# Optimization experiments

Measured on AMD Instinct MI355X. Metric: run time of the kernel, lower is better.

Reference implementation:

```python
import jax, jax.numpy as jnp
import numpy as np

N, DIM_IN, DIM_V, VH, VW, H = 2048, 256, 256, 7, 7, 64
NK = VH * VW
DIM_Q = DIM_V * H  # 16384
EPS = 1e-5


def layer_norm(x, g, b):
    m = jnp.mean(x, axis=-1, keepdims=True)
    var = jnp.mean((x - m) ** 2, axis=-1, keepdims=True)
    return (x - m) / jnp.sqrt(var + EPS) * g + b


def setup_inputs() -> dict:
    key = jax.random.key(0)
    ks = jax.random.split(key, 6)
    x = jax.random.normal(ks[0], (N, DIM_IN), dtype=jnp.float32)
    v = jax.random.normal(ks[1], (N, DIM_V, NK), dtype=jnp.float32)
    Wq_w = jax.random.normal(ks[2], (2 * DIM_Q, DIM_IN), dtype=jnp.float32) * 0.02
    Wq_b = jnp.zeros((2 * DIM_Q,), dtype=jnp.float32)
    Wv_w = jax.random.normal(ks[3], (DIM_IN, DIM_V * NK), dtype=jnp.float32) * 0.02
    Wv_b = jnp.zeros((DIM_IN,), dtype=jnp.float32)
    return {
        "x": x, "v": v,
        "Wq_w": Wq_w, "Wq_b": Wq_b,
        "ln0_g": jnp.ones((H,), jnp.float32), "ln0_b": jnp.zeros((H,), jnp.float32),
        "ln1_g": jnp.ones((DIM_V,), jnp.float32), "ln1_b": jnp.zeros((DIM_V,), jnp.float32),
        "Wv_w": Wv_w, "Wv_b": Wv_b,
        "lnv_g": jnp.ones((DIM_IN,), jnp.float32), "lnv_b": jnp.zeros((DIM_IN,), jnp.float32),
        "lnf_g": jnp.ones((DIM_IN,), jnp.float32), "lnf_b": jnp.zeros((DIM_IN,), jnp.float32),
    }


def reference(x, v, Wq_w, Wq_b, ln0_g, ln0_b, ln1_g, ln1_b, Wv_w, Wv_b, lnv_g, lnv_b, lnf_g, lnf_b):
    n = x.shape[0]
    vt = jnp.transpose(v, (0, 2, 1))                      # [N, Nk, V]
    q = x @ Wq_w.T + Wq_b                                 # [N, 2*dim_q]
    # dynamic_conv_num == 2: two bmm stages with per-sample weights from q
    p1 = q[:, :DIM_Q].reshape(n, DIM_V, H)                # [N, V, H]
    t = jnp.einsum('nkv,nvh->nkh', vt, p1)                # [N, Nk, H]
    t = jax.nn.relu(layer_norm(t, ln0_g, ln0_b))
    p2 = q[:, DIM_Q:].reshape(n, H, DIM_V)                # [N, H, V]
    t = jnp.einsum('nkh,nhv->nkv', t, p2)                 # [N, Nk, V]
    t = jax.nn.relu(layer_norm(t, ln1_g, ln1_b))
    flat = t.reshape(n, NK * DIM_V)                       # [N, Nk*V]
    w = jax.nn.relu(layer_norm(flat @ Wv_w.T + Wv_b, lnv_g, lnv_b))  # [N, dim_in]
    return layer_norm(x + w, lnf_g, lnf_b)
```

## Files before the change

kernel.cpp:

```cpp
#include <hip/hip_runtime.h>

#define LN_EPS 1e-5f


typedef __attribute__((ext_vector_type(8))) short short8;
typedef __attribute__((ext_vector_type(16))) float f32x16;

__global__ __launch_bounds__(256) void k0_split(
    const float* __restrict__ in, ushort* __restrict__ hi,
    ushort* __restrict__ lo, int n4)
{
    const int i = blockIdx.x * 256 + threadIdx.x;
    if (i >= n4) return;
    const float4 f = ((const float4*)in)[i];
    const uint ux = __float_as_uint(f.x), uy = __float_as_uint(f.y);
    const uint uz = __float_as_uint(f.z), uw = __float_as_uint(f.w);
    ushort4 h, l;
    h.x = (ushort)(ux >> 16); h.y = (ushort)(uy >> 16);
    h.z = (ushort)(uz >> 16); h.w = (ushort)(uw >> 16);
    l.x = (ushort)(__float_as_uint(f.x - __uint_as_float(ux & 0xffff0000u)) >> 16);
    l.y = (ushort)(__float_as_uint(f.y - __uint_as_float(uy & 0xffff0000u)) >> 16);
    l.z = (ushort)(__float_as_uint(f.z - __uint_as_float(uz & 0xffff0000u)) >> 16);
    l.w = (ushort)(__float_as_uint(f.w - __uint_as_float(uw & 0xffff0000u)) >> 16);
    ((ushort4*)hi)[i] = h;
    ((ushort4*)lo)[i] = l;
}

template<bool HAS_BIAS>
__global__ __launch_bounds__(256, 2) void gemm_sb3(
    const ushort* __restrict__ Ah, const ushort* __restrict__ Al,
    const float* __restrict__ B, const float* __restrict__ bias,
    float* __restrict__ C, int lda, int ldb, int ldc,
    size_t cSplitStride, int kPerSplit)
{
    __shared__ __align__(16) ushort sAh[8192];
    __shared__ __align__(16) ushort sAl[8192];
    __shared__ __align__(16) ushort sBh[8192];
    __shared__ __align__(16) ushort sBl[8192];

    const int tid = threadIdx.x;
    const int m0 = blockIdx.x << 7;
    const int j0 = blockIdx.y << 7;
    const int ks0 = blockIdx.z * kPerSplit;
    float* Cb = C + (size_t)blockIdx.z * cSplitStride;

    const int lane = tid & 63;
    const int wid = tid >> 6;
    const int wr = wid >> 1;
    const int wc = wid & 1;
    const int swz = (lane & 7) << 3;
    const int rA = (wr << 6) + (lane & 31);
    const int rB = (wc << 6) + (lane & 31);
    const int khalf = (lane >> 5) << 3;

    f32x16 acc[2][2];
#pragma unroll
    for (int r = 0; r < 2; ++r)
#pragma unroll
        for (int c = 0; c < 2; ++c)
#pragma unroll
            for (int e = 0; e < 16; ++e) acc[r][c][e] = 0.f;

    for (int kg0 = 0; kg0 < kPerSplit; kg0 += 64) {
        const int kg = ks0 + kg0;

        uint4 av[8];
#pragma unroll
        for (int p = 0; p < 2; ++p) {
            const ushort* src = p ? Al : Ah;
#pragma unroll
            for (int i = 0; i < 4; ++i) {
                const int id = tid + (i << 8);
                const int row = id >> 3;
                const int c8 = (id & 7) << 3;
                av[p * 4 + i] = *(const uint4*)(src + (size_t)(m0 + row) * lda + kg + c8);
            }
        }
        float4 bv[8];
#pragma unroll
        for (int i = 0; i < 8; ++i) {
            const int id = tid + (i << 8);
            const int row = id >> 4;
            const int c4 = (id & 15) << 2;
            bv[i] = *(const float4*)(B + (size_t)(j0 + row) * ldb + kg + c4);
        }

        if (kg0 > 0) __syncthreads();

#pragma unroll
        for (int p = 0; p < 2; ++p) {
            ushort* dst = p ? sAl : sAh;
#pragma unroll
            for (int i = 0; i < 4; ++i) {
                const int id = tid + (i << 8);
                const int row = id >> 3;
                const int c8 = (id & 7) << 3;
                *(uint4*)&dst[((row << 6) + c8) ^ ((row & 7) << 3)] = av[p * 4 + i];
            }
        }
#pragma unroll
        for (int i = 0; i < 8; ++i) {
            const int id = tid + (i << 8);
            const int row = id >> 4;
            const int c4 = (id & 15) << 2;
            const uint ux = __float_as_uint(bv[i].x), uy = __float_as_uint(bv[i].y);
            const uint uz = __float_as_uint(bv[i].z), uw = __float_as_uint(bv[i].w);
            const float lx = bv[i].x - __uint_as_float(ux & 0xffff0000u);
            const float ly = bv[i].y - __uint_as_float(uy & 0xffff0000u);
            const float lz = bv[i].z - __uint_as_float(uz & 0xffff0000u);
            const float lw = bv[i].w - __uint_as_float(uw & 0xffff0000u);
            const uint h01 = (ux >> 16) | (uy & 0xffff0000u);
            const uint h23 = (uz >> 16) | (uw & 0xffff0000u);
            const uint l01 = (__float_as_uint(lx) >> 16) | (__float_as_uint(ly) & 0xffff0000u);
            const uint l23 = (__float_as_uint(lz) >> 16) | (__float_as_uint(lw) & 0xffff0000u);
            const int sidx = ((row << 6) + c4) ^ ((row & 7) << 3);
            *(uint2*)&sBh[sidx] = make_uint2(h01, h23);
            *(uint2*)&sBl[sidx] = make_uint2(l01, l23);
        }
        __syncthreads();

#pragma unroll
        for (int ks = 0; ks < 4; ++ks) {
            const int kf = (ks << 4) + khalf;
            const int ia0 = ((rA << 6) + kf) ^ swz;
            const int ia1 = (((rA + 32) << 6) + kf) ^ swz;
            const int ib0 = ((rB << 6) + kf) ^ swz;
            const int ib1 = (((rB + 32) << 6) + kf) ^ swz;
            const short8 a0h = *(const short8*)&sAh[ia0];
            const short8 a0l = *(const short8*)&sAl[ia0];
            const short8 a1h = *(const short8*)&sAh[ia1];
            const short8 a1l = *(const short8*)&sAl[ia1];
            const short8 b0h = *(const short8*)&sBh[ib0];
            const short8 b0l = *(const short8*)&sBl[ib0];
            const short8 b1h = *(const short8*)&sBh[ib1];
            const short8 b1l = *(const short8*)&sBl[ib1];

            acc[0][0] = __builtin_amdgcn_mfma_f32_32x32x16_bf16(a0h, b0h, acc[0][0], 0, 0, 0);
            acc[0][1] = __builtin_amdgcn_mfma_f32_32x32x16_bf16(a0h, b1h, acc[0][1], 0, 0, 0);
            acc[1][0] = __builtin_amdgcn_mfma_f32_32x32x16_bf16(a1h, b0h, acc[1][0], 0, 0, 0);
            acc[1][1] = __builtin_amdgcn_mfma_f32_32x32x16_bf16(a1h, b1h, acc[1][1], 0, 0, 0);
            acc[0][0] = __builtin_amdgcn_mfma_f32_32x32x16_bf16(a0h, b0l, acc[0][0], 0, 0, 0);
            acc[0][1] = __builtin_amdgcn_mfma_f32_32x32x16_bf16(a0h, b1l, acc[0][1], 0, 0, 0);
            acc[1][0] = __builtin_amdgcn_mfma_f32_32x32x16_bf16(a1h, b0l, acc[1][0], 0, 0, 0);
            acc[1][1] = __builtin_amdgcn_mfma_f32_32x32x16_bf16(a1h, b1l, acc[1][1], 0, 0, 0);
            acc[0][0] = __builtin_amdgcn_mfma_f32_32x32x16_bf16(a0l, b0h, acc[0][0], 0, 0, 0);
            acc[0][1] = __builtin_amdgcn_mfma_f32_32x32x16_bf16(a0l, b1h, acc[0][1], 0, 0, 0);
            acc[1][0] = __builtin_amdgcn_mfma_f32_32x32x16_bf16(a1l, b0h, acc[1][0], 0, 0, 0);
            acc[1][1] = __builtin_amdgcn_mfma_f32_32x32x16_bf16(a1l, b1h, acc[1][1], 0, 0, 0);
        }
    }

#pragma unroll
    for (int rb = 0; rb < 2; ++rb)
#pragma unroll
        for (int cb = 0; cb < 2; ++cb) {
            const int col = j0 + (wc << 6) + (cb << 5) + (lane & 31);
            const float bvv = HAS_BIAS ? bias[col] : 0.0f;
            const int rbase = m0 + (wr << 6) + (rb << 5) + ((lane >> 5) << 2);
            float* cp = Cb + (size_t)rbase * ldc + col;
#pragma unroll
            for (int reg = 0; reg < 16; ++reg) {
                const int rr = (reg & 3) + ((reg >> 2) << 3);
                cp[(size_t)rr * ldc] = acc[rb][cb][reg] + bvv;
            }
        }
}

__global__ __launch_bounds__(1024, 4) void k2_dynconv(
    const float* __restrict__ v, const float* __restrict__ q,
    const float* __restrict__ ln0g, const float* __restrict__ ln0b,
    const float* __restrict__ ln1g, const float* __restrict__ ln1b,
    ushort* __restrict__ fhi, ushort* __restrict__ flo)
{
    __shared__ __align__(16) float sm[33028];
    float* const vL = sm;
    float* const pL = sm + 13312;
    float* const tL = sm + 29696;

    const int n = blockIdx.x;
    const int tid = threadIdx.x;
    const float* vrow = v + (size_t)n * 12544;
    const float* qrow = q + (size_t)n * 32768;

    float4 rp2[4];
#pragma unroll
    for (int j = 0; j < 4; ++j)
        rp2[j] = *(const float4*)(qrow + 16384 + ((tid + j * 1024) << 2));

#pragma unroll
    for (int j = 0; j < 4; ++j) {
        const int c = tid + j * 1024;
        *(float4*)&pL[c << 2] = *(const float4*)(qrow + (c << 2));
    }
#pragma unroll
    for (int j = 0; j < 4; ++j) {
        const int c = tid + j * 1024;
        if (c < 3136) {
            const float4 f = *(const float4*)(vrow + (c << 2));
            const int i0 = c << 2;
#pragma unroll
            for (int e = 0; e < 4; ++e) {
                const int i = i0 + e;
                const int dv = (int)(((uint)i * 85599u) >> 22);
                const int k = i - dv * 49;
                vL[dv * 52 + k] = ((const float*)&f)[e];
            }
        }
    }
    __syncthreads();

    float ta[4][4];
    const int ktA = tid >> 4;
    const int h0A = (tid & 15) << 2;
    if (tid < 208) {
#pragma unroll
        for (int r = 0; r < 4; ++r)
#pragma unroll
            for (int c = 0; c < 4; ++c) ta[r][c] = 0.f;
        int aoff[4];
#pragma unroll
        for (int r = 0; r < 4; ++r) {
            const int k = (ktA << 2) + r;
            aoff[r] = (k < 49 ? k : 48) * 52;
        }
#pragma unroll 2
        for (int dv = 0; dv < 256; dv += 1) {
            const float4 b4 = *(const float4*)&pL[(dv << 6) + h0A];
            const float* bp = (const float*)&b4;
            float a[4];
#pragma unroll
            for (int r = 0; r < 4; ++r) a[r] = vL[dv * 52 + ((ktA << 2) + r < 49 ? (ktA << 2) + r : 48)];
#pragma unroll
            for (int r = 0; r < 4; ++r)
#pragma unroll
                for (int c = 0; c < 4; ++c)
                    ta[r][c] = fmaf(a[r], bp[c], ta[r][c]);
        }
        (void)aoff;
    }
    __syncthreads();

#pragma unroll
    for (int j = 0; j < 4; ++j)
        *(float4*)&pL[(tid + j * 1024) << 2] = rp2[j];

    if (tid < 208) {
        float s1[4], s2[4];
#pragma unroll
        for (int r = 0; r < 4; ++r) {
            s1[r] = ta[r][0] + ta[r][1] + ta[r][2] + ta[r][3];
            s2[r] = ta[r][0]*ta[r][0] + ta[r][1]*ta[r][1]
                  + ta[r][2]*ta[r][2] + ta[r][3]*ta[r][3];
        }
#pragma unroll
        for (int m = 1; m < 16; m <<= 1)
#pragma unroll
            for (int r = 0; r < 4; ++r) {
                s1[r] += __shfl_xor(s1[r], m);
                s2[r] += __shfl_xor(s2[r], m);
            }
        const float4 g4 = *(const float4*)&ln0g[h0A];
        const float4 b4 = *(const float4*)&ln0b[h0A];
        const float* gp = (const float*)&g4;
        const float* bp = (const float*)&b4;
#pragma unroll
        for (int r = 0; r < 4; ++r) {
            const int k = (ktA << 2) + r;
            if (k < 49) {
                const float mean = s1[r] * (1.f / 64.f);
                const float var = s2[r] * (1.f / 64.f) - mean * mean;
                const float rstd = rsqrtf(var + LN_EPS);
                float4 o;
                o.x = fmaxf((ta[r][0] - mean) * rstd * gp[0] + bp[0], 0.f);
                o.y = fmaxf((ta[r][1] - mean) * rstd * gp[1] + bp[1], 0.f);
                o.z = fmaxf((ta[r][2] - mean) * rstd * gp[2] + bp[2], 0.f);
                o.w = fmaxf((ta[r][3] - mean) * rstd * gp[3] + bp[3], 0.f);
                *(float4*)&tL[k * 68 + h0A] = o;
            }
        }
    }
    __syncthreads();

    if (tid < 416) {
        const int ktB = tid >> 5;
        const int j0B = (tid & 31) << 3;
        int roff[4];
#pragma unroll
        for (int r = 0; r < 4; ++r) {
            const int k = (ktB << 2) + r;
            roff[r] = (k < 49 ? k : 48) * 68;
        }
        float acc[4][8];
#pragma unroll
        for (int r = 0; r < 4; ++r)
#pragma unroll
            for (int c = 0; c < 8; ++c) acc[r][c] = 0.f;

        for (int hb = 0; hb < 16; ++hb) {
            float4 a4[4];
#pragma unroll
            for (int r = 0; r < 4; ++r)
                a4[r] = *(const float4*)&tL[roff[r] + (hb << 2)];
#pragma unroll
            for (int hh = 0; hh < 4; ++hh) {
                const int h = (hb << 2) + hh;
                const float4 b0 = *(const float4*)&pL[(h << 8) + j0B];
                const float4 b1 = *(const float4*)&pL[(h << 8) + j0B + 4];
                const float* bp0 = (const float*)&b0;
                const float* bp1 = (const float*)&b1;
#pragma unroll
                for (int r = 0; r < 4; ++r) {
                    const float a = ((const float*)&a4[r])[hh];
#pragma unroll
                    for (int c = 0; c < 4; ++c) {
                        acc[r][c]     = fmaf(a, bp0[c], acc[r][c]);
                        acc[r][c + 4] = fmaf(a, bp1[c], acc[r][c + 4]);
                    }
                }
            }
        }

        float s1[4], s2[4];
#pragma unroll
        for (int r = 0; r < 4; ++r) {
            float a1 = 0.f, a2 = 0.f;
#pragma unroll
            for (int c = 0; c < 8; ++c) { a1 += acc[r][c]; a2 += acc[r][c] * acc[r][c]; }
            s1[r] = a1; s2[r] = a2;
        }
#pragma unroll
        for (int m = 1; m < 32; m <<= 1)
#pragma unroll
            for (int r = 0; r < 4; ++r) {
                s1[r] += __shfl_xor(s1[r], m);
                s2[r] += __shfl_xor(s2[r], m);
            }
        const float4 g0 = *(const float4*)&ln1g[j0B];
        const float4 g1 = *(const float4*)&ln1g[j0B + 4];
        const float4 bb0 = *(const float4*)&ln1b[j0B];
        const float4 bb1 = *(const float4*)&ln1b[j0B + 4];
        const float* gp = (const float*)&g0;
        const float* gq = (const float*)&g1;
        const float* bp = (const float*)&bb0;
        const float* bq = (const float*)&bb1;
#pragma unroll
        for (int r = 0; r < 4; ++r) {
            const int k = (ktB << 2) + r;
            if (k < 49) {
                const float mean = s1[r] * (1.f / 256.f);
                const float var = s2[r] * (1.f / 256.f) - mean * mean;
                const float rstd = rsqrtf(var + LN_EPS);
                float o[8];
#pragma unroll
                for (int c = 0; c < 4; ++c) {
                    o[c]     = fmaxf((acc[r][c]     - mean) * rstd * gp[c] + bp[c], 0.f);
                    o[c + 4] = fmaxf((acc[r][c + 4] - mean) * rstd * gq[c] + bq[c], 0.f);
                }
                ushort4 h4a, h4b, l4a, l4b;
#pragma unroll
                for (int c = 0; c < 4; ++c) {
                    const uint u = __float_as_uint(o[c]);
                    ((ushort*)&h4a)[c] = (ushort)(u >> 16);
                    ((ushort*)&l4a)[c] = (ushort)(__float_as_uint(o[c] - __uint_as_float(u & 0xffff0000u)) >> 16);
                    const uint u2 = __float_as_uint(o[c + 4]);
                    ((ushort*)&h4b)[c] = (ushort)(u2 >> 16);
                    ((ushort*)&l4b)[c] = (ushort)(__float_as_uint(o[c + 4] - __uint_as_float(u2 & 0xffff0000u)) >> 16);
                }
                const size_t fo = (size_t)n * 12544 + k * 256 + j0B;
                *(ushort4*)&fhi[fo] = h4a;
                *(ushort4*)&fhi[fo + 4] = h4b;
                *(ushort4*)&flo[fo] = l4a;
                *(ushort4*)&flo[fo + 4] = l4b;
            }
        }
    }
}

__global__ __launch_bounds__(256) void k4_final(
    const float* __restrict__ wpart, const float* __restrict__ x,
    const float* __restrict__ Wvb,
    const float* __restrict__ lnvg, const float* __restrict__ lnvb,
    const float* __restrict__ lnfg, const float* __restrict__ lnfb,
    float* __restrict__ out)
{
    const int n = (blockIdx.x << 2) + (threadIdx.x >> 6);
    const int lane = threadIdx.x & 63;
    const int j = lane << 2;

    float a0 = 0.f, a1 = 0.f, a2 = 0.f, a3 = 0.f;
#pragma unroll
    for (int s = 0; s < 14; ++s) {
        const float4 p = *(const float4*)&wpart[((size_t)s * 2048 + n) * 256 + j];
        a0 += p.x; a1 += p.y; a2 += p.z; a3 += p.w;
    }
    const float4 bb = *(const float4*)&Wvb[j];
    a0 += bb.x; a1 += bb.y; a2 += bb.z; a3 += bb.w;

    float s1 = a0 + a1 + a2 + a3;
    float s2 = a0*a0 + a1*a1 + a2*a2 + a3*a3;
#pragma unroll
    for (int off = 32; off > 0; off >>= 1) {
        s1 += __shfl_xor(s1, off);
        s2 += __shfl_xor(s2, off);
    }
    float m = s1 * (1.f / 256.f);
    float var = s2 * (1.f / 256.f) - m * m;
    float rr = rsqrtf(var + LN_EPS);
    const float4 g = *(const float4*)&lnvg[j];
    const float4 b = *(const float4*)&lnvb[j];
    const float w0 = fmaxf((a0 - m) * rr * g.x + b.x, 0.f);
    const float w1 = fmaxf((a1 - m) * rr * g.y + b.y, 0.f);
    const float w2 = fmaxf((a2 - m) * rr * g.z + b.z, 0.f);
    const float w3 = fmaxf((a3 - m) * rr * g.w + b.w, 0.f);

    const float4 xv = *(const float4*)&x[(size_t)n * 256 + j];
    const float t0 = xv.x + w0, t1 = xv.y + w1, t2 = xv.z + w2, t3 = xv.w + w3;
    s1 = t0 + t1 + t2 + t3;
    s2 = t0*t0 + t1*t1 + t2*t2 + t3*t3;
#pragma unroll
    for (int off = 32; off > 0; off >>= 1) {
        s1 += __shfl_xor(s1, off);
        s2 += __shfl_xor(s2, off);
    }
    m = s1 * (1.f / 256.f);
    var = s2 * (1.f / 256.f) - m * m;
    rr = rsqrtf(var + LN_EPS);
    const float4 gf = *(const float4*)&lnfg[j];
    const float4 bf = *(const float4*)&lnfb[j];
    float4 o;
    o.x = (t0 - m) * rr * gf.x + bf.x;
    o.y = (t1 - m) * rr * gf.y + bf.y;
    o.z = (t2 - m) * rr * gf.z + bf.z;
    o.w = (t3 - m) * rr * gf.w + bf.w;
    *(float4*)&out[(size_t)n * 256 + j] = o;
}

extern "C" void kernel_launch(void* const* d_in, const int* in_sizes, int n_in,
                              void* d_out, int out_size, void* d_ws, size_t ws_size,
                              hipStream_t stream)
{
    const float* x    = (const float*)d_in[0];
    const float* v    = (const float*)d_in[1];
    const float* Wq_w = (const float*)d_in[2];
    const float* Wq_b = (const float*)d_in[3];
    const float* ln0g = (const float*)d_in[4];
    const float* ln0b = (const float*)d_in[5];
    const float* ln1g = (const float*)d_in[6];
    const float* ln1b = (const float*)d_in[7];
    const float* Wv_w = (const float*)d_in[8];
    const float* Wv_b = (const float*)d_in[9];
    const float* lnvg = (const float*)d_in[10];
    const float* lnvb = (const float*)d_in[11];
    const float* lnfg = (const float*)d_in[12];
    const float* lnfb = (const float*)d_in[13];
    float* out = (float*)d_out;

    if (ws_size < 371195904ull) return;
    char* ws = (char*)d_ws;
    float* q        = (float*)ws;
    ushort* flat_hi = (ushort*)(ws + 268435456u);
    ushort* flat_lo = (ushort*)(ws + 319815680u);
    ushort* xs_hi   = (ushort*)(ws + 268435456u);
    ushort* xs_lo   = xs_hi + 524288;
    float* wpart    = q;

    k0_split<<<512, 256, 0, stream>>>(x, xs_hi, xs_lo, 131072);

    gemm_sb3<true><<<dim3(16, 256, 1), 256, 0, stream>>>(
        xs_hi, xs_lo, Wq_w, Wq_b, q, 256, 256, 32768, 0, 256);

    k2_dynconv<<<2048, 1024, 0, stream>>>(v, q, ln0g, ln0b, ln1g, ln1b,
                                          flat_hi, flat_lo);

    gemm_sb3<false><<<dim3(16, 2, 14), 256, 0, stream>>>(
        flat_hi, flat_lo, Wv_w, nullptr, wpart, 12544, 12544, 256,
        (size_t)2048 * 256, 896);

    k4_final<<<512, 256, 0, stream>>>(wpart, x, Wv_b, lnvg, lnvb, lnfg, lnfb, out);
}
```

Baseline: 893.2 us.

## Stream dynconv operands through LDS in chunks to shrink shared memory and block size

The per-sample dynamic conv kernel now loads v and the two q weight slices in four chunks of 64 rows each instead of staging everything at once. This cuts LDS from about 132KB to about 43KB per block and halves the block to 512 threads, so more blocks can reside per CU. The first stage now reads vL as a float4, and the second stage's weight tile uses an XOR-swizzled layout to avoid bank conflicts. In exchange there are extra barriers per chunk, and less load latency overlaps within a block.

```diff
diff --git a/kernel.cpp b/kernel.cpp
--- a/kernel.cpp
+++ b/kernel.cpp
@@ -166,83 +166,62 @@
         }
 }
 
-__global__ __launch_bounds__(1024, 4) void k2_dynconv(
+__global__ __launch_bounds__(512, 4) void k2_dynconv(
     const float* __restrict__ v, const float* __restrict__ q,
     const float* __restrict__ ln0g, const float* __restrict__ ln0b,
     const float* __restrict__ ln1g, const float* __restrict__ ln1b,
     ushort* __restrict__ fhi, ushort* __restrict__ flo)
 {
-    __shared__ __align__(16) float sm[33028];
-    float* const vL = sm;
-    float* const pL = sm + 13312;
-    float* const tL = sm + 29696;
+    __shared__ __align__(16) float sm[10756];
+    float* const thL = sm;
+    float* const vL  = sm + 3332;
+    float* const pL  = sm + 6660;
 
     const int n = blockIdx.x;
     const int tid = threadIdx.x;
     const float* vrow = v + (size_t)n * 12544;
     const float* qrow = q + (size_t)n * 32768;
 
-    float4 rp2[4];
-#pragma unroll
-    for (int j = 0; j < 4; ++j)
-        rp2[j] = *(const float4*)(qrow + 16384 + ((tid + j * 1024) << 2));
-
-#pragma unroll
-    for (int j = 0; j < 4; ++j) {
-        const int c = tid + j * 1024;
-        *(float4*)&pL[c << 2] = *(const float4*)(qrow + (c << 2));
-    }
-#pragma unroll
-    for (int j = 0; j < 4; ++j) {
-        const int c = tid + j * 1024;
-        if (c < 3136) {
-            const float4 f = *(const float4*)(vrow + (c << 2));
-            const int i0 = c << 2;
-#pragma unroll
-            for (int e = 0; e < 4; ++e) {
-                const int i = i0 + e;
-                const int dv = (int)(((uint)i * 85599u) >> 22);
-                const int k = i - dv * 49;
-                vL[dv * 52 + k] = ((const float*)&f)[e];
-            }
-        }
-    }
-    __syncthreads();
-
-    float ta[4][4];
     const int ktA = tid >> 4;
     const int h0A = (tid & 15) << 2;
-    if (tid < 208) {
-#pragma unroll
-        for (int r = 0; r < 4; ++r)
-#pragma unroll
-            for (int c = 0; c < 4; ++c) ta[r][c] = 0.f;
-        int aoff[4];
-#pragma unroll
-        for (int r = 0; r < 4; ++r) {
-            const int k = (ktA << 2) + r;
-            aoff[r] = (k < 49 ? k : 48) * 52;
-        }
+    float ta[4][4];
+#pragma unroll
+    for (int r = 0; r < 4; ++r)
+#pragma unroll
+        for (int c = 0; c < 4; ++c) ta[r][c] = 0.f;
+
+    for (int ch = 0; ch < 4; ++ch) {
+        if (ch) __syncthreads();
+        for (int i4 = tid; i4 < 784; i4 += 512) {
+            const float4 f = *(const float4*)(vrow + ch * 3136 + (i4 << 2));
+            const int base = i4 << 2;
+#pragma unroll
+            for (int e = 0; e < 4; ++e) {
+                const int idx = base + e;
+                const int dv = (int)(((uint)idx * 85599u) >> 22);
+                const int k = idx - dv * 49;
+                vL[dv * 52 + k] = ((const float*)&f)[e];
+            }
+        }
+        for (int i = tid; i < 1024; i += 512)
+            *(float4*)&pL[i << 2] = *(const float4*)(qrow + (ch << 12) + (i << 2));
+        __syncthreads();
+
+        if (tid < 208) {
 #pragma unroll 2
-        for (int dv = 0; dv < 256; dv += 1) {
-            const float4 b4 = *(const float4*)&pL[(dv << 6) + h0A];
-            const float* bp = (const float*)&b4;
-            float a[4];
-#pragma unroll
-            for (int r = 0; r < 4; ++r) a[r] = vL[dv * 52 + ((ktA << 2) + r < 49 ? (ktA << 2) + r : 48)];
-#pragma unroll
-            for (int r = 0; r < 4; ++r)
-#pragma unroll
-                for (int c = 0; c < 4; ++c)
-                    ta[r][c] = fmaf(a[r], bp[c], ta[r][c]);
-        }
-        (void)aoff;
-    }
-    __syncthreads();
-
-#pragma unroll
-    for (int j = 0; j < 4; ++j)
-        *(float4*)&pL[(tid + j * 1024) << 2] = rp2[j];
+            for (int dv = 0; dv < 64; ++dv) {
+                const float4 a4 = *(const float4*)&vL[dv * 52 + (ktA << 2)];
+                const float4 b4 = *(const float4*)&pL[(dv << 6) + h0A];
+                const float* ap = (const float*)&a4;
+                const float* bp = (const float*)&b4;
+#pragma unroll
+                for (int r = 0; r < 4; ++r)
+#pragma unroll
+                    for (int c = 0; c < 4; ++c)
+                        ta[r][c] = fmaf(ap[r], bp[c], ta[r][c]);
+            }
+        }
+    }
 
     if (tid < 208) {
         float s1[4], s2[4];
@@ -275,51 +254,69 @@
                 o.y = fmaxf((ta[r][1] - mean) * rstd * gp[1] + bp[1], 0.f);
                 o.z = fmaxf((ta[r][2] - mean) * rstd * gp[2] + bp[2], 0.f);
                 o.w = fmaxf((ta[r][3] - mean) * rstd * gp[3] + bp[3], 0.f);
-                *(float4*)&tL[k * 68 + h0A] = o;
+                *(float4*)&thL[k * 68 + h0A] = o;
             }
         }
     }
     __syncthreads();
 
-    if (tid < 416) {
-        const int ktB = tid >> 5;
-        const int j0B = (tid & 31) << 3;
-        int roff[4];
-#pragma unroll
-        for (int r = 0; r < 4; ++r) {
-            const int k = (ktB << 2) + r;
-            roff[r] = (k < 49 ? k : 48) * 68;
-        }
-        float acc[4][8];
-#pragma unroll
-        for (int r = 0; r < 4; ++r)
-#pragma unroll
-            for (int c = 0; c < 8; ++c) acc[r][c] = 0.f;
-
-        for (int hb = 0; hb < 16; ++hb) {
-            float4 a4[4];
-#pragma unroll
-            for (int r = 0; r < 4; ++r)
-                a4[r] = *(const float4*)&tL[roff[r] + (hb << 2)];
-#pragma unroll
-            for (int hh = 0; hh < 4; ++hh) {
-                const int h = (hb << 2) + hh;
-                const float4 b0 = *(const float4*)&pL[(h << 8) + j0B];
-                const float4 b1 = *(const float4*)&pL[(h << 8) + j0B + 4];
-                const float* bp0 = (const float*)&b0;
-                const float* bp1 = (const float*)&b1;
-#pragma unroll
-                for (int r = 0; r < 4; ++r) {
-                    const float a = ((const float*)&a4[r])[hh];
-#pragma unroll
-                    for (int c = 0; c < 4; ++c) {
-                        acc[r][c]     = fmaf(a, bp0[c], acc[r][c]);
-                        acc[r][c + 4] = fmaf(a, bp1[c], acc[r][c + 4]);
+    const int ktB = tid >> 5;
+    const int j0B = (tid & 31) << 3;
+    const int g0 = (tid & 31) << 1;
+    const int sw0 = (g0 ^ (g0 >> 3)) << 2;
+    const int sw1 = ((g0 + 1) ^ ((g0 + 1) >> 3)) << 2;
+    int roffB[4];
+#pragma unroll
+    for (int r = 0; r < 4; ++r) {
+        const int k = (ktB << 2) + r;
+        roffB[r] = (k < 49 ? k : 48) * 68;
+    }
+    float acc[4][8];
+#pragma unroll
+    for (int r = 0; r < 4; ++r)
+#pragma unroll
+        for (int c = 0; c < 8; ++c) acc[r][c] = 0.f;
+
+    for (int ch = 0; ch < 4; ++ch) {
+        if (ch) __syncthreads();
+        for (int i = tid; i < 1024; i += 512) {
+            const int h = i >> 6;
+            const int g = i & 63;
+            const int s = g ^ (g >> 3);
+            *(float4*)&pL[(h << 8) + (s << 2)] =
+                *(const float4*)(qrow + 16384 + (ch << 12) + (i << 2));
+        }
+        __syncthreads();
+
+        if (tid < 416) {
+#pragma unroll
+            for (int hb = 0; hb < 4; ++hb) {
+                float4 a4[4];
+#pragma unroll
+                for (int r = 0; r < 4; ++r)
+                    a4[r] = *(const float4*)&thL[roffB[r] + (ch << 4) + (hb << 2)];
+#pragma unroll
+                for (int hh = 0; hh < 4; ++hh) {
+                    const int hl = (hb << 2) + hh;
+                    const float4 b0 = *(const float4*)&pL[(hl << 8) + sw0];
+                    const float4 b1 = *(const float4*)&pL[(hl << 8) + sw1];
+                    const float* bp0 = (const float*)&b0;
+                    const float* bp1 = (const float*)&b1;
+#pragma unroll
+                    for (int r = 0; r < 4; ++r) {
+                        const float a = ((const float*)&a4[r])[hh];
+#pragma unroll
+                        for (int c = 0; c < 4; ++c) {
+                            acc[r][c]     = fmaf(a, bp0[c], acc[r][c]);
+                            acc[r][c + 4] = fmaf(a, bp1[c], acc[r][c + 4]);
+                        }
                     }
                 }
             }
         }
-
+    }
+
+    if (tid < 416) {
         float s1[4], s2[4];
 #pragma unroll
         for (int r = 0; r < 4; ++r) {
@@ -335,14 +332,14 @@
                 s1[r] += __shfl_xor(s1[r], m);
                 s2[r] += __shfl_xor(s2[r], m);
             }
-        const float4 g0 = *(const float4*)&ln1g[j0B];
-        const float4 g1 = *(const float4*)&ln1g[j0B + 4];
-        const float4 bb0 = *(const float4*)&ln1b[j0B];
-        const float4 bb1 = *(const float4*)&ln1b[j0B + 4];
-        const float* gp = (const float*)&g0;
-        const float* gq = (const float*)&g1;
-        const float* bp = (const float*)&bb0;
-        const float* bq = (const float*)&bb1;
+        const float4 g0v = *(const float4*)&ln1g[j0B];
+        const float4 g1v = *(const float4*)&ln1g[j0B + 4];
+        const float4 b0v = *(const float4*)&ln1b[j0B];
+        const float4 b1v = *(const float4*)&ln1b[j0B + 4];
+        const float* gp = (const float*)&g0v;
+        const float* gq = (const float*)&g1v;
+        const float* bp = (const float*)&b0v;
+        const float* bq = (const float*)&b1v;
 #pragma unroll
         for (int r = 0; r < 4; ++r) {
             const int k = (ktB << 2) + r;
@@ -469,8 +466,8 @@
     gemm_sb3<true><<<dim3(16, 256, 1), 256, 0, stream>>>(
         xs_hi, xs_lo, Wq_w, Wq_b, q, 256, 256, 32768, 0, 256);
 
-    k2_dynconv<<<2048, 1024, 0, stream>>>(v, q, ln0g, ln0b, ln1g, ln1b,
-                                          flat_hi, flat_lo);
+    k2_dynconv<<<2048, 512, 0, stream>>>(v, q, ln0g, ln0b, ln1g, ln1b,
+                                         flat_hi, flat_lo);
 
     gemm_sb3<false><<<dim3(16, 2, 14), 256, 0, stream>>>(
         flat_hi, flat_lo, Wv_w, nullptr, wpart, 12544, 12544, 256,
```

New measurement: 803.4 us. 1.11x faster.
